# Optimization experiments

Measured on AMD Instinct MI355X. Metric: run time of the kernel, lower is better.

Reference implementation:

```python
import jax, jax.numpy as jnp
import numpy as np

EMB = 768
HEADS = 8
HEAD = EMB // HEADS  # 96


def setup_inputs() -> dict:
    key = jax.random.key(0)
    k1, k2, k3, k4 = jax.random.split(key, 4)
    B, S = 16, 2048
    x = jax.random.normal(k1, (B, S, EMB), dtype=jnp.float32)
    # torch nn.Linear(in=EMB, out=HEAD, bias=False); store transposed [EMB, HEAD]
    scale = 1.0 / np.sqrt(EMB)
    Wq = jax.random.uniform(k2, (EMB, HEAD), jnp.float32, -scale, scale)
    Wk = jax.random.uniform(k3, (EMB, HEAD), jnp.float32, -scale, scale)
    Wv = jax.random.uniform(k4, (EMB, HEAD), jnp.float32, -scale, scale)
    return {"x": x, "Wq": Wq, "Wk": Wk, "Wv": Wv}


def reference(x, Wq, Wk, Wv):
    # x: [B, S, E]
    q = x @ Wq  # [B, S, H]
    k = x @ Wk
    v = x @ Wv
    S = x.shape[1]
    # scores: [B, S, S], scaled by head_size**-0.5
    weights = jnp.einsum('bqh,bkh->bqk', q, k) * (k.shape[-1] ** -0.5)
    causal = jnp.tril(jnp.ones((S, S), dtype=bool))
    masked = jnp.where(causal, weights, jnp.float32(-1e20))
    attn = jax.nn.softmax(masked, axis=-1)
    # dropout is identity at inference
    out = jnp.einsum('bqk,bkh->bqh', attn, v)  # [B, S, H]
    return out
```

## Files before the change

### kernel.cpp

```cpp
#include <hip/hip_runtime.h>
#include <math.h>

#define EMB_K   768
#define NH      96
#define SEQLEN  2048
#define NBATCH  16
#define MROWS   (NBATCH * SEQLEN)

typedef __bf16 v8bf __attribute__((ext_vector_type(8)));
typedef float  v4f  __attribute__((ext_vector_type(4)));

#define QSCALE (0.10206207261596575f * 1.4426950408889634f)

#if __has_builtin(__builtin_amdgcn_global_load_lds)
#define ASYNC_LDS 1
#else
#define ASYNC_LDS 0
#endif

__global__ __launch_bounds__(256) void pack_w(
    const float* __restrict__ Wq,
    const float* __restrict__ Wk,
    const float* __restrict__ Wv,
    __bf16* __restrict__ Wp)
{
    int t = blockIdx.x * 256 + threadIdx.x;
    if (t >= 3 * 24 * 6 * 64) return;
    int l  = t & 63;
    int fj = (t >> 6) % 6;
    int s  = ((t >> 6) / 6) % 24;
    int w  = (t >> 6) / (6 * 24);
    const float* W = (w == 0) ? Wq : ((w == 1) ? Wk : Wv);
    int n     = fj * 16 + (l & 15);
    int kbase = s * 32 + (l >> 4) * 8;
    __bf16 o[8];
    #pragma unroll
    for (int e = 0; e < 8; ++e)
        o[e] = (__bf16)W[(size_t)(kbase + e) * NH + n];
    *(v8bf*)(Wp + (size_t)t * 8) = *(v8bf*)o;
}

__device__ inline v8bf cvt8(const float4& a, const float4& b)
{
    v8bf r;
    r[0] = (__bf16)a.x; r[1] = (__bf16)a.y; r[2] = (__bf16)a.z; r[3] = (__bf16)a.w;
    r[4] = (__bf16)b.x; r[5] = (__bf16)b.y; r[6] = (__bf16)b.z; r[7] = (__bf16)b.w;
    return r;
}

__global__ __launch_bounds__(256) void qkv_fused(
    const float* __restrict__ x,
    const __bf16* __restrict__ Wp,
    __bf16* __restrict__ qk,
    __bf16* __restrict__ vt)
{
    __shared__ __bf16 Bs[2][18][512];
    __shared__ __bf16 VsT[96][72];

    const int wave = threadIdx.x >> 6;
    const int lane = threadIdx.x & 63;
    const int mlow = lane & 15;
    const int kq   = lane >> 4;
    const int m0   = blockIdx.x * 64;
    const int r0   = m0 + wave * 16;

    const float* xr = x + (size_t)(r0 + mlow) * EMB_K + kq * 8;

    v4f acc[3][6];
    #pragma unroll
    for (int w = 0; w < 3; ++w)
        #pragma unroll
        for (int j = 0; j < 6; ++j)
            acc[w][j] = (v4f)0.0f;

    auto stage = [&](int s, int buf) {
        for (int f = wave; f < 18; f += 4) {
            const __bf16* src = Wp + ((size_t)((f / 6) * 24 + s) * 6 + (f % 6)) * 512
                                   + (size_t)lane * 8;
#if ASYNC_LDS
            __builtin_amdgcn_global_load_lds(
                (const __attribute__((address_space(1))) void*)src,
                (__attribute__((address_space(3))) void*)&Bs[buf][f][0],
                16, 0, 0);
#else
            *(v8bf*)&Bs[buf][f][(size_t)lane * 8] = *(const v8bf*)src;
#endif
        }
    };

    stage(0, 0);
    float4 plo = *(const float4*)(xr);
    float4 phi = *(const float4*)(xr + 4);
    __syncthreads();

    for (int s = 0; s < 24; ++s) {
        const int cur = s & 1;
        if (s < 23) stage(s + 1, cur ^ 1);
        const int sn = (s < 23) ? s + 1 : 23;
        float4 nlo = *(const float4*)(xr + sn * 32);
        float4 nhi = *(const float4*)(xr + sn * 32 + 4);

        v8bf a = cvt8(plo, phi);
        #pragma unroll
        for (int w = 0; w < 3; ++w)
            #pragma unroll
            for (int j = 0; j < 6; ++j) {
                v8bf bf = *(const v8bf*)&Bs[cur][w * 6 + j][(size_t)lane * 8];
                acc[w][j] = __builtin_amdgcn_mfma_f32_16x16x32_bf16(a, bf, acc[w][j], 0, 0, 0);
            }
        plo = nlo; phi = nhi;
        __syncthreads();
    }

    #pragma unroll
    for (int w = 0; w < 2; ++w) {
        __bf16* op = qk + (size_t)w * MROWS * NH;
        const float sc = (w == 0) ? QSCALE : 1.0f;
        #pragma unroll
        for (int j = 0; j < 6; ++j)
            #pragma unroll
            for (int r = 0; r < 4; ++r)
                op[(size_t)(r0 + kq * 4 + r) * NH + j * 16 + mlow] =
                    (__bf16)(acc[w][j][r] * sc);
    }
    #pragma unroll
    for (int j = 0; j < 6; ++j)
        #pragma unroll
        for (int r = 0; r < 4; ++r)
            VsT[j * 16 + mlow][wave * 16 + kq * 4 + r] = (__bf16)acc[2][j][r];
    __syncthreads();
    #pragma unroll
    for (int it = 0; it < 3; ++it) {
        int idx = it * 256 + threadIdx.x;
        int c = idx >> 3, g = idx & 7;
        *(v8bf*)(vt + (size_t)c * MROWS + m0 + g * 8) = *(const v8bf*)&VsT[c][g * 8];
    }
}

__device__ const unsigned char JTAB[30] = {
    20, 24, 28, 32, 36, 40, 44, 45, 48, 49, 52, 53, 56, 57, 60, 61,
    0, 4, 8, 12, 16, 25, 29, 33, 37, 41, 50, 54, 58, 62
};

__global__ __launch_bounds__(256, 2) void attn_mfma(
    const __bf16* __restrict__ qk,
    const __bf16* __restrict__ vt,
    float* __restrict__ out,
    __bf16* __restrict__ Opart,
    float* __restrict__ ml)
{
    __shared__ __bf16 Kf[2][12][512];
    __shared__ __bf16 Vf[2][12][512];
    __shared__ __bf16 Ps[4][16][72];

    const int bid = blockIdx.x;
    const int b   = bid & 15;
    const int j   = bid >> 4;
    const int enc = JTAB[j];
    const int qt  = enc >> 2;
    const int c0  = enc & 3;
    const int ntiles = 2 * qt + 2;
    const int t0  = c0 * 12;
    const int t1  = (t0 + 12 < ntiles) ? (t0 + 12) : ntiles;
    const int nch = (ntiles + 11) / 12;

    const int wave = threadIdx.x >> 6;
    const int lane = threadIdx.x & 63;
    const int mlow = lane & 15;
    const int kq   = lane >> 4;
    const int qw0  = qt * 128 + wave * 32;

    const __bf16* qp  = qk + (size_t)b * SEQLEN * NH;
    const __bf16* kp  = qk + (size_t)MROWS * NH + (size_t)b * SEQLEN * NH;
    const __bf16* vtp = vt + (size_t)b * SEQLEN;

    v8bf qa[2][3];
    #pragma unroll
    for (int g2 = 0; g2 < 2; ++g2)
        #pragma unroll
        for (int s = 0; s < 3; ++s)
            qa[g2][s] = *(const v8bf*)(qp + (size_t)(qw0 + g2 * 16 + mlow) * NH
                                          + s * 32 + kq * 8);

    v4f lsum[2];
    v4f O[2][6];
    #pragma unroll
    for (int g2 = 0; g2 < 2; ++g2) {
        lsum[g2] = (v4f)0.0f;
        #pragma unroll
        for (int jj = 0; jj < 6; ++jj) O[g2][jj] = (v4f)0.0f;
    }

    auto stage = [&](int t, int buf) {
        const int k0 = t * 64;
        #pragma unroll
        for (int i = 0; i < 6; ++i) {
            const int f = wave * 6 + i;
            const __bf16* src;
            __bf16* dst;
            if (f < 12) {
                const int t4 = f / 3, s = f - t4 * 3;
                src = kp + (size_t)(k0 + t4 * 16 + mlow) * NH + s * 32 + kq * 8;
                dst = &Kf[buf][f][0];
            } else {
                const int fv = f - 12;
                const int jj = fv >> 1, h = fv & 1;
                src = vtp + (size_t)(jj * 16 + mlow) * MROWS + k0 + h * 32 + kq * 8;
                dst = &Vf[buf][fv][0];
            }
#if ASYNC_LDS
            __builtin_amdgcn_global_load_lds(
                (const __attribute__((address_space(1))) void*)src,
                (__attribute__((address_space(3))) void*)dst,
                16, 0, 0);
#else
            *(v8bf*)(dst + (size_t)lane * 8) = *(const v8bf*)src;
#endif
        }
    };

    stage(t0, 0);
    __syncthreads();

    for (int t = t0; t < t1; ++t) {
        const int buf = (t - t0) & 1;
        if (t + 1 < t1) stage(t + 1, buf ^ 1);
        const int k0 = t * 64;

        if (k0 <= qw0 + 31) {
            const bool msk = (k0 + 63 > qw0);
            #pragma unroll
            for (int g2 = 0; g2 < 2; ++g2) {
                float s2[4][4];
                #pragma unroll
                for (int t4 = 0; t4 < 4; ++t4) {
                    v4f sa = (v4f)0.0f;
                    #pragma unroll
                    for (int s = 0; s < 3; ++s) {
                        v8bf kb = *(const v8bf*)&Kf[buf][t4 * 3 + s][(size_t)lane * 8];
                        sa = __builtin_amdgcn_mfma_f32_16x16x32_bf16(qa[g2][s], kb, sa, 0, 0, 0);
                    }
                    #pragma unroll
                    for (int r = 0; r < 4; ++r) s2[t4][r] = sa[r];
                }
                if (msk) {
                    #pragma unroll
                    for (int t4 = 0; t4 < 4; ++t4)
                        #pragma unroll
                        for (int r = 0; r < 4; ++r)
                            if (k0 + t4 * 16 + mlow > qw0 + g2 * 16 + kq * 4 + r)
                                s2[t4][r] = -1e20f;
                }

                v4f pvv[4];
                #pragma unroll
                for (int t4 = 0; t4 < 4; ++t4)
                    #pragma unroll
                    for (int r = 0; r < 4; ++r)
                        pvv[t4][r] = exp2f(s2[t4][r]);
                lsum[g2] += (pvv[0] + pvv[1]) + (pvv[2] + pvv[3]);

                #pragma unroll
                for (int t4 = 0; t4 < 4; ++t4)
                    #pragma unroll
                    for (int r = 0; r < 4; ++r)
                        Ps[wave][kq * 4 + r][t4 * 16 + mlow] = (__bf16)pvv[t4][r];

                v8bf pa0 = *(const v8bf*)&Ps[wave][mlow][kq * 8];
                v8bf pa1 = *(const v8bf*)&Ps[wave][mlow][32 + kq * 8];

                #pragma unroll
                for (int jj = 0; jj < 6; ++jj) {
                    v8bf vb0 = *(const v8bf*)&Vf[buf][jj * 2][(size_t)lane * 8];
                    v8bf vb1 = *(const v8bf*)&Vf[buf][jj * 2 + 1][(size_t)lane * 8];
                    O[g2][jj] = __builtin_amdgcn_mfma_f32_16x16x32_bf16(pa0, vb0, O[g2][jj], 0, 0, 0);
                    O[g2][jj] = __builtin_amdgcn_mfma_f32_16x16x32_bf16(pa1, vb1, O[g2][jj], 0, 0, 0);
                }
            }
        }
        __syncthreads();
    }

    #pragma unroll
    for (int off = 1; off < 16; off <<= 1)
        #pragma unroll
        for (int g2 = 0; g2 < 2; ++g2)
            #pragma unroll
            for (int r = 0; r < 4; ++r)
                lsum[g2][r] += __shfl_xor(lsum[g2][r], off);

    if (nch == 1) {
        #pragma unroll
        for (int g2 = 0; g2 < 2; ++g2)
            #pragma unroll
            for (int r = 0; r < 4; ++r) {
                float inv = 1.0f / lsum[g2][r];
                float* orow = out + ((size_t)b * SEQLEN + qw0 + g2 * 16 + kq * 4 + r) * NH;
                #pragma unroll
                for (int jj = 0; jj < 6; ++jj)
                    orow[jj * 16 + mlow] = O[g2][jj][r] * inv;
            }
    } else {
        const int e = (b * 10 + (qt - 6)) * 3 + c0;
        __bf16* Pp = Opart + (size_t)e * 12288;
        #pragma unroll
        for (int g2 = 0; g2 < 2; ++g2)
            #pragma unroll
            for (int r = 0; r < 4; ++r) {
                const int row = wave * 32 + g2 * 16 + kq * 4 + r;
                float inv = 1.0f / lsum[g2][r];
                #pragma unroll
                for (int jj = 0; jj < 6; ++jj)
                    Pp[row * 96 + jj * 16 + mlow] = (__bf16)(O[g2][jj][r] * inv);
                if (mlow == 0) {
                    ml[(size_t)e * 256 + row * 2]     = 0.0f;
                    ml[(size_t)e * 256 + row * 2 + 1] = lsum[g2][r];
                }
            }
    }
}

__global__ __launch_bounds__(256) void attn_combine(
    const __bf16* __restrict__ Opart,
    const float* __restrict__ ml,
    float* __restrict__ out)
{
    __shared__ float wsh[3][128];
    const int b   = blockIdx.x & 15;
    const int qr  = blockIdx.x >> 4;
    const int qt  = 6 + qr;
    const int nch = (qt >= 12) ? 3 : 2;
    const int e0  = (b * 10 + qr) * 3;
    const int tid = threadIdx.x;

    if (tid < 128) {
        float m[3], l[3];
        float M = -INFINITY;
        #pragma unroll
        for (int c = 0; c < 3; ++c) {
            if (c < nch) {
                m[c] = ml[(size_t)(e0 + c) * 256 + tid * 2];
                l[c] = ml[(size_t)(e0 + c) * 256 + tid * 2 + 1];
            } else { m[c] = -INFINITY; l[c] = 0.0f; }
            M = fmaxf(M, m[c]);
        }
        float a[3], s = 0.0f;
        #pragma unroll
        for (int c = 0; c < 3; ++c) { a[c] = exp2f(m[c] - M) * l[c]; s += a[c]; }
        float inv = 1.0f / s;
        #pragma unroll
        for (int c = 0; c < 3; ++c) wsh[c][tid] = a[c] * inv;
    }
    __syncthreads();

    float* op = out + ((size_t)b * SEQLEN + (size_t)qt * 128) * NH;
    #pragma unroll
    for (int it = 0; it < 6; ++it) {
        int idx = it * 256 + tid;
        int row = idx / 12;
        int off = idx * 8;
        float acc[8];
        #pragma unroll
        for (int k = 0; k < 8; ++k) acc[k] = 0.0f;
        #pragma unroll
        for (int c = 0; c < 3; ++c) {
            if (c < nch) {
                v8bf p = *(const v8bf*)(Opart + (size_t)(e0 + c) * 12288 + off);
                float w = wsh[c][row];
                #pragma unroll
                for (int k = 0; k < 8; ++k) acc[k] += w * (float)p[k];
            }
        }
        *(float4*)(op + off)     = make_float4(acc[0], acc[1], acc[2], acc[3]);
        *(float4*)(op + off + 4) = make_float4(acc[4], acc[5], acc[6], acc[7]);
    }
}

extern "C" void kernel_launch(void* const* d_in, const int* in_sizes, int n_in,
                              void* d_out, int out_size, void* d_ws, size_t ws_size,
                              hipStream_t stream)
{
    (void)in_sizes; (void)n_in; (void)out_size; (void)ws_size;
    const float* x  = (const float*)d_in[0];
    const float* Wq = (const float*)d_in[1];
    const float* Wk = (const float*)d_in[2];
    const float* Wv = (const float*)d_in[3];
    float* out = (float*)d_out;

    __bf16* qk    = (__bf16*)d_ws;
    __bf16* vt    = qk + (size_t)2 * MROWS * NH;
    __bf16* Wp    = vt + (size_t)NH * MROWS;
    __bf16* Opart = Wp + (size_t)3 * 24 * 6 * 512;
    float*  ml    = (float*)(Opart + (size_t)480 * 12288);

    pack_w<<<(3 * 24 * 6 * 64 + 255) / 256, 256, 0, stream>>>(Wq, Wk, Wv, Wp);
    qkv_fused<<<MROWS / 64, 256, 0, stream>>>(x, Wp, qk, vt);
    attn_mfma<<<dim3(480), 256, 0, stream>>>(qk, vt, out, Opart, ml);
    attn_combine<<<dim3(160), 256, 0, stream>>>(Opart, ml, out);
}
```

Measured before the change: 220.4 us.

## Stage weights through registers and double-buffer x loads in QKV projection

Replaces the async global-to-LDS weight staging with register-staged loads that are issued before the MFMA loop and written to the other LDS buffer afterwards. Prefetches x two k-steps ahead using a two-slot register buffer, and adds an occupancy hint of 3 blocks per SM. The goal is to hide global load latency behind the MFMA work. The cost is more register pressure, and the launch bound may force spills.

```diff
diff --git a/kernel.cpp b/kernel.cpp
--- a/kernel.cpp
+++ b/kernel.cpp
@@ -48,7 +48,7 @@
     return r;
 }
 
-__global__ __launch_bounds__(256) void qkv_fused(
+__global__ __launch_bounds__(256, 3) void qkv_fused(
     const float* __restrict__ x,
     const __bf16* __restrict__ Wp,
     __bf16* __restrict__ qk,
@@ -66,6 +66,8 @@
 
     const float* xr = x + (size_t)(r0 + mlow) * EMB_K + kq * 8;
 
+    const int nf = (wave < 2) ? 5 : 4;
+
     v4f acc[3][6];
     #pragma unroll
     for (int w = 0; w < 3; ++w)
@@ -73,34 +75,44 @@
         for (int j = 0; j < 6; ++j)
             acc[w][j] = (v4f)0.0f;
 
-    auto stage = [&](int s, int buf) {
-        for (int f = wave; f < 18; f += 4) {
-            const __bf16* src = Wp + ((size_t)((f / 6) * 24 + s) * 6 + (f % 6)) * 512
-                                   + (size_t)lane * 8;
-#if ASYNC_LDS
-            __builtin_amdgcn_global_load_lds(
-                (const __attribute__((address_space(1))) void*)src,
-                (__attribute__((address_space(3))) void*)&Bs[buf][f][0],
-                16, 0, 0);
-#else
-            *(v8bf*)&Bs[buf][f][(size_t)lane * 8] = *(const v8bf*)src;
-#endif
-        }
-    };
-
-    stage(0, 0);
-    float4 plo = *(const float4*)(xr);
-    float4 phi = *(const float4*)(xr + 4);
+    v8bf btmp[5];
+    #pragma unroll
+    for (int i = 0; i < 5; ++i)
+        if (i < nf) {
+            const int f = wave + 4 * i;
+            btmp[i] = *(const v8bf*)(Wp + ((size_t)((f / 6) * 24) * 6 + (f % 6)) * 512
+                                        + (size_t)lane * 8);
+        }
+    float4 xreg[2][2];
+    xreg[0][0] = *(const float4*)(xr);
+    xreg[0][1] = *(const float4*)(xr + 4);
+    xreg[1][0] = *(const float4*)(xr + 32);
+    xreg[1][1] = *(const float4*)(xr + 36);
+    #pragma unroll
+    for (int i = 0; i < 5; ++i)
+        if (i < nf)
+            *(v8bf*)&Bs[0][wave + 4 * i][(size_t)lane * 8] = btmp[i];
     __syncthreads();
 
     for (int s = 0; s < 24; ++s) {
         const int cur = s & 1;
-        if (s < 23) stage(s + 1, cur ^ 1);
-        const int sn = (s < 23) ? s + 1 : 23;
-        float4 nlo = *(const float4*)(xr + sn * 32);
-        float4 nhi = *(const float4*)(xr + sn * 32 + 4);
-
-        v8bf a = cvt8(plo, phi);
+
+        v8bf a = cvt8(xreg[cur][0], xreg[cur][1]);
+
+        if (s < 23) {
+            #pragma unroll
+            for (int i = 0; i < 5; ++i)
+                if (i < nf) {
+                    const int f = wave + 4 * i;
+                    btmp[i] = *(const v8bf*)(Wp + ((size_t)((f / 6) * 24 + (s + 1)) * 6
+                                                   + (f % 6)) * 512 + (size_t)lane * 8);
+                }
+        }
+        if (s < 22) {
+            xreg[cur][0] = *(const float4*)(xr + (s + 2) * 32);
+            xreg[cur][1] = *(const float4*)(xr + (s + 2) * 32 + 4);
+        }
+
         #pragma unroll
         for (int w = 0; w < 3; ++w)
             #pragma unroll
@@ -108,7 +120,13 @@
                 v8bf bf = *(const v8bf*)&Bs[cur][w * 6 + j][(size_t)lane * 8];
                 acc[w][j] = __builtin_amdgcn_mfma_f32_16x16x32_bf16(a, bf, acc[w][j], 0, 0, 0);
             }
-        plo = nlo; phi = nhi;
+
+        if (s < 23) {
+            #pragma unroll
+            for (int i = 0; i < 5; ++i)
+                if (i < nf)
+                    *(v8bf*)&Bs[cur ^ 1][wave + 4 * i][(size_t)lane * 8] = btmp[i];
+        }
         __syncthreads();
     }
 
```

After: 223.5 us. Within noise of the previous version (+1.4%).
